# Kernel optimization log

Hardware: AMD Instinct MI355X
Metric: run time of the kernel (lower is better)

Reference implementation:

```python
import jax, jax.numpy as jnp
import numpy as np


def _apply_1q_batched(state, gate, q):
    # state: (B,2,2,2,2) complex; gate: (B,2,2) complex; acts on qubit q
    state = jnp.moveaxis(state, q + 1, -1)
    state = jnp.einsum('bij,b...j->b...i', gate, state)
    return jnp.moveaxis(state, -1, q + 1)


def _apply_cnot(state, c, t):
    # flip target bit where control bit == 1
    s0, s1 = jnp.split(state, 2, axis=c + 1)
    s1 = jnp.flip(s1, axis=t + 1)
    return jnp.concatenate([s0, s1], axis=c + 1)


def _quantum_features(angles, params):
    # angles: (B,4) RY rotation angles; params: (4,) RZ angles
    B = angles.shape[0]
    state = jnp.zeros((B, 16), jnp.complex64).at[:, 0].set(1.0).reshape(B, 2, 2, 2, 2)
    # RY(x_i) on each wire (batched angle per sample)
    for q in range(4):
        th = 0.5 * angles[:, q]
        c, s = jnp.cos(th), jnp.sin(th)
        gate = jnp.stack([jnp.stack([c, -s], -1), jnp.stack([s, c], -1)], -2).astype(jnp.complex64)
        state = _apply_1q_batched(state, gate, q)
    # RZ(params[i]) on wire i followed by CNOT(i, (i+1)%4), interleaved as in source
    pc = params.astype(jnp.complex64)
    for q in range(4):
        ph = jnp.exp(jnp.array([-0.5j, 0.5j], jnp.complex64) * pc[q])
        shp = [1, 1, 1, 1, 1]
        shp[q + 1] = 2
        state = state * ph.reshape(shp)
        state = _apply_cnot(state, q, (q + 1) % 4)
    probs = state.real ** 2 + state.imag ** 2  # (B,2,2,2,2)
    feats = []
    for q in range(4):
        axes = tuple(a for a in range(1, 5) if a != q + 1)
        p = probs.sum(axes)  # (B,2)
        feats.append(p[:, 0] - p[:, 1])  # <Z_q>
    return jnp.stack(feats, -1)  # (B,4)


def _deconv2x2(x, w, b):
    # PyTorch ConvTranspose2d with kernel=stride=2, padding=0 (non-overlapping)
    # x: (B,Ci,H,W), w: (Ci,Co,2,2), b: (Co,)
    B, Ci, H, W = x.shape
    Co = w.shape[1]
    y = jnp.einsum('bchw,codk->bohdwk', x, w).reshape(B, Co, 2 * H, 2 * W)
    return y + b[None, :, None, None]


def setup_inputs() -> dict:
    key = jax.random.key(0)
    ks = jax.random.split(key, 10)
    B = 16384
    return {
        'x': jax.random.uniform(ks[0], (B, 1, 28, 28), jnp.float32),
        'var_params': jax.random.normal(ks[1], (4,), jnp.float32),
        'w_lat': jax.random.normal(ks[2], (224, 4), jnp.float32) * 0.3,
        'b_lat': jax.random.normal(ks[3], (224,), jnp.float32) * 0.05,
        'w_fc': jax.random.normal(ks[4], (392, 224), jnp.float32) * 0.05,
        'b_fc': jax.random.normal(ks[5], (392,), jnp.float32) * 0.05,
        'w_d1': jax.random.normal(ks[6], (8, 4, 2, 2), jnp.float32) * 0.2,
        'b_d1': jax.random.normal(ks[7], (4,), jnp.float32) * 0.05,
        'w_d2': jax.random.normal(ks[8], (4, 1, 2, 2), jnp.float32) * 0.2,
        'b_d2': jax.random.normal(ks[9], (1,), jnp.float32) * 0.05,
    }


def reference(x, var_params, w_lat, b_lat, w_fc, b_fc, w_d1, b_d1, w_d2, b_d2):
    # quadrant means -> 4 angles per sample
    quad = jnp.stack([
        x[:, 0, :14, :14].mean((1, 2)),
        x[:, 0, :14, 14:].mean((1, 2)),
        x[:, 0, 14:, :14].mean((1, 2)),
        x[:, 0, 14:, 14:].mean((1, 2)),
    ], axis=1)  # (B,4)
    qf = _quantum_features(quad, var_params)  # (B,4)
    latent = jax.nn.relu(qf @ w_lat.T + b_lat)  # (B,224)
    h = jax.nn.relu(latent @ w_fc.T + b_fc)  # (B,392)
    h = h.reshape(-1, 8, 7, 7)
    h = jax.nn.relu(_deconv2x2(h, w_d1, b_d1))  # (B,4,14,14)
    out = jax.nn.sigmoid(_deconv2x2(h, w_d2, b_d2))  # (B,1,28,28)
    return out
```

## Files before the change

kernel.cpp:

```cpp
#include <hip/hip_runtime.h>
#include <math.h>

#define G 16
#define HS 396
#define LSTR 232

typedef __attribute__((ext_vector_type(8))) __bf16 bf16x8;
typedef __attribute__((ext_vector_type(4))) float f32x4;
typedef __attribute__((ext_vector_type(2))) float f32x2;

__global__ void wconv_kernel(const float* __restrict__ w_fc, __bf16* __restrict__ wb) {
  int tile = blockIdx.x;
  int kt   = blockIdx.y;
  int lane = threadIdx.x;
  int n  = tile * 16 + (lane & 15);
  int k0 = kt * 32 + (lane >> 4) * 8;
  bf16x8 v;
  if (n < 392) {
    const float* src = w_fc + (size_t)n * 224 + k0;
    float4 f0 = *(const float4*)(src);
    float4 f1 = *(const float4*)(src + 4);
    v[0] = (__bf16)f0.x; v[1] = (__bf16)f0.y; v[2] = (__bf16)f0.z; v[3] = (__bf16)f0.w;
    v[4] = (__bf16)f1.x; v[5] = (__bf16)f1.y; v[6] = (__bf16)f1.z; v[7] = (__bf16)f1.w;
  } else {
    #pragma unroll
    for (int j = 0; j < 8; ++j) v[j] = (__bf16)0.f;
  }
  *(bf16x8*)(wb + ((size_t)(tile * 7 + kt) * 64 + lane) * 8) = v;
}

__global__ __launch_bounds__(256, 4) void fused_kernel(
    const float* __restrict__ x, const float* __restrict__ params,
    const __bf16* __restrict__ wb,
    const float* __restrict__ w_lat, const float* __restrict__ b_lat,
    const float* __restrict__ b_fc,
    const float* __restrict__ w_d1, const float* __restrict__ b_d1,
    const float* __restrict__ w_d2, const float* __restrict__ b_d2,
    float* __restrict__ out, int B)
{
  __shared__ __align__(16) __bf16 latb[G * LSTR];
  __shared__ __align__(16) float hbuf[G * HS];
  __shared__ float qfs[G * 4];
  __shared__ float wd1[128];
  __shared__ float wd2[16];
  __shared__ float bd1[4];
  const int t = threadIdx.x;
  const int wv = t >> 6;
  const int lane = t & 63;
  const int s0g = blockIdx.x * G;
  if (s0g >= B) return;

  if (t < 128) wd1[t] = w_d1[t];
  else if (t < 144) wd2[t - 128] = w_d2[t - 128];
  else if (t < 148) bd1[t - 144] = b_d1[t - 144];

  {
    const float* xb = x + (size_t)(s0g + wv * 4) * 784;
    float acc[4][4];
    #pragma unroll
    for (int i = 0; i < 4; ++i)
      #pragma unroll
      for (int q = 0; q < 4; ++q) acc[i][q] = 0.f;
    for (int i4 = lane; i4 < 196; i4 += 64) {
      int base = i4 * 4;
      int r = base / 28;
      int cb = base - r * 28;
      float bt = (r >= 14) ? 1.f : 0.f;
      float tp = 1.f - bt;
      float w0[4], w1[4], w2[4], w3[4];
      #pragma unroll
      for (int e = 0; e < 4; ++e) {
        float lf = ((cb + e) < 14) ? 1.f : 0.f;
        float rf = 1.f - lf;
        w0[e] = tp * lf; w1[e] = tp * rf; w2[e] = bt * lf; w3[e] = bt * rf;
      }
      #pragma unroll
      for (int smp = 0; smp < 4; ++smp) {
        f32x4 v = __builtin_nontemporal_load((const f32x4*)(xb + smp * 784 + base));
        #pragma unroll
        for (int e = 0; e < 4; ++e) {
          acc[smp][0] = fmaf(v[e], w0[e], acc[smp][0]);
          acc[smp][1] = fmaf(v[e], w1[e], acc[smp][1]);
          acc[smp][2] = fmaf(v[e], w2[e], acc[smp][2]);
          acc[smp][3] = fmaf(v[e], w3[e], acc[smp][3]);
        }
      }
    }
    #pragma unroll
    for (int smp = 0; smp < 4; ++smp)
      #pragma unroll
      for (int q = 0; q < 4; ++q)
        #pragma unroll
        for (int o = 32; o > 0; o >>= 1)
          acc[smp][q] += __shfl_down(acc[smp][q], o, 64);
    if (lane == 0) {
      const float inv = 1.f / 196.f;
      #pragma unroll
      for (int smp = 0; smp < 4; ++smp) {
        float4 o;
        o.x = acc[smp][0] * inv; o.y = acc[smp][1] * inv;
        o.z = acc[smp][2] * inv; o.w = acc[smp][3] * inv;
        *(float4*)(qfs + (wv * 4 + smp) * 4) = o;
      }
    }
  }
  __syncthreads();

  if (t < G) {
    float means[4] = {qfs[t * 4], qfs[t * 4 + 1], qfs[t * 4 + 2], qfs[t * 4 + 3]};
    float cs[4], sn[4];
    #pragma unroll
    for (int q = 0; q < 4; ++q) {
      float th = 0.5f * means[q];
      sn[q] = __sinf(th);
      cs[q] = __cosf(th);
    }
    float re[16], im[16];
    #pragma unroll
    for (int idx = 0; idx < 16; ++idx) {
      float a = ((idx >> 3) & 1) ? sn[0] : cs[0];
      a *= ((idx >> 2) & 1) ? sn[1] : cs[1];
      a *= ((idx >> 1) & 1) ? sn[2] : cs[2];
      a *= (idx & 1) ? sn[3] : cs[3];
      re[idx] = a;
      im[idx] = 0.f;
    }
    #pragma unroll
    for (int q = 0; q < 4; ++q) {
      float hp = 0.5f * params[q];
      float sp = __sinf(hp), cp = __cosf(hp);
      int qb = 3 - q;
      #pragma unroll
      for (int idx = 0; idx < 16; ++idx) {
        float sg = ((idx >> qb) & 1) ? sp : -sp;
        float r0 = re[idx], i0 = im[idx];
        re[idx] = r0 * cp - i0 * sg;
        im[idx] = r0 * sg + i0 * cp;
      }
      int cm = 1 << qb;
      int tm = 1 << (3 - ((q + 1) & 3));
      #pragma unroll
      for (int idx = 0; idx < 16; ++idx) {
        if ((idx & cm) && !(idx & tm)) {
          int j = idx | tm;
          float tr = re[idx]; re[idx] = re[j]; re[j] = tr;
          float ti = im[idx]; im[idx] = im[j]; im[j] = ti;
        }
      }
    }
    #pragma unroll
    for (int q = 0; q < 4; ++q) {
      int qb = 3 - q;
      float z = 0.f;
      #pragma unroll
      for (int idx = 0; idx < 16; ++idx) {
        float p = re[idx] * re[idx] + im[idx] * im[idx];
        z += ((idx >> qb) & 1) ? -p : p;
      }
      qfs[t * 4 + q] = z;
    }
  }
  __syncthreads();

  for (int v = t; v < G * 224; v += 256) {
    int s = v / 224;
    int j = v - s * 224;
    float4 w = *(const float4*)(w_lat + j * 4);
    float a = b_lat[j];
    a = fmaf(qfs[s * 4 + 0], w.x, a);
    a = fmaf(qfs[s * 4 + 1], w.y, a);
    a = fmaf(qfs[s * 4 + 2], w.z, a);
    a = fmaf(qfs[s * 4 + 3], w.w, a);
    latb[s * LSTR + j] = (__bf16)fmaxf(a, 0.f);
  }
  __syncthreads();

  {
    const int m = lane & 15;
    const int kq = lane >> 4;
    const __bf16* arow = latb + m * LSTR + kq * 8;
    for (int tile = wv; tile < 25; tile += 4) {
      f32x4 acc = {0.f, 0.f, 0.f, 0.f};
      const bf16x8* bp = (const bf16x8*)(wb + ((size_t)(tile * 7) * 64 + lane) * 8);
      #pragma unroll
      for (int kt = 0; kt < 7; ++kt) {
        bf16x8 a = *(const bf16x8*)(arow + kt * 32);
        bf16x8 b = bp[kt * 64];
        acc = __builtin_amdgcn_mfma_f32_16x16x32_bf16(a, b, acc, 0, 0, 0);
      }
      int j = tile * 16 + m;
      if (j < 392) {
        float bf = b_fc[j];
        #pragma unroll
        for (int r = 0; r < 4; ++r)
          hbuf[(kq * 4 + r) * HS + j] = fmaxf(acc[r] + bf, 0.f);
      }
    }
  }
  __syncthreads();

  const float bd2v = b_d2[0];
  for (int v = t; v < G * 196; v += 256) {
    int s = v / 196;
    int p = v - s * 196;
    int Y = p / 14;
    int X = p - Y * 14;
    int y = Y >> 1, ey = Y & 1, xx = X >> 1, ex = X & 1;
    const float* hs = hbuf + s * HS + y * 7 + xx;
    float hv[8];
    #pragma unroll
    for (int ci = 0; ci < 8; ++ci) hv[ci] = hs[ci * 49];
    float o1[4];
    #pragma unroll
    for (int co = 0; co < 4; ++co) {
      float a = bd1[co];
      #pragma unroll
      for (int ci = 0; ci < 8; ++ci)
        a = fmaf(hv[ci], wd1[ci * 16 + co * 4 + ey * 2 + ex], a);
      o1[co] = fmaxf(a, 0.f);
    }
    size_t basep = (size_t)(s0g + s) * 784;
    #pragma unroll
    for (int dy = 0; dy < 2; ++dy) {
      float v0 = bd2v, v1 = bd2v;
      #pragma unroll
      for (int co = 0; co < 4; ++co) {
        v0 = fmaf(o1[co], wd2[co * 4 + dy * 2 + 0], v0);
        v1 = fmaf(o1[co], wd2[co * 4 + dy * 2 + 1], v1);
      }
      f32x2 o;
      o[0] = 1.f / (1.f + __expf(-v0));
      o[1] = 1.f / (1.f + __expf(-v1));
      __builtin_nontemporal_store(o, (f32x2*)(out + basep + (size_t)(2 * Y + dy) * 28 + 2 * X));
    }
  }
}

extern "C" void kernel_launch(void* const* d_in, const int* in_sizes, int n_in,
                              void* d_out, int out_size, void* d_ws, size_t ws_size,
                              hipStream_t stream) {
  const float* x          = (const float*)d_in[0];
  const float* var_params = (const float*)d_in[1];
  const float* w_lat      = (const float*)d_in[2];
  const float* b_lat      = (const float*)d_in[3];
  const float* w_fc       = (const float*)d_in[4];
  const float* b_fc       = (const float*)d_in[5];
  const float* w_d1       = (const float*)d_in[6];
  const float* b_d1       = (const float*)d_in[7];
  const float* w_d2       = (const float*)d_in[8];
  const float* b_d2       = (const float*)d_in[9];
  float* out = (float*)d_out;

  __bf16* wb = (__bf16*)d_ws;

  int B = in_sizes[0] / 784;
  wconv_kernel<<<dim3(25, 7), 64, 0, stream>>>(w_fc, wb);
  fused_kernel<<<(B + G - 1) / G, 256, 0, stream>>>(
      x, var_params, wb, w_lat, b_lat, b_fc, w_d1, b_d1, w_d2, b_d2, out, B);
}
```

Before: 143.9 us.

## Parallelize quantum sim across lanes, drop barriers, store hidden as bf16

Simulates the 4-qubit circuit with 16 lanes per sample: one amplitude per lane, CNOTs done as shuffles and expectations as xor-reductions. Previously only 16 threads did this serially. Each wave now handles its own 4 samples end to end through the latent layer, which removes two block-wide barriers. The hidden buffer becomes bf16 and launch bounds rise to 6 blocks per CU, cutting LDS use to raise occupancy. This costs some precision in the deconvolution inputs and may force register spills under the tighter bound.

```diff
diff --git a/kernel.cpp b/kernel.cpp
--- a/kernel.cpp
+++ b/kernel.cpp
@@ -2,7 +2,7 @@
 #include <math.h>
 
 #define G 16
-#define HS 396
+#define HS2 400
 #define LSTR 232
 
 typedef __attribute__((ext_vector_type(8))) __bf16 bf16x8;
@@ -29,7 +29,7 @@
   *(bf16x8*)(wb + ((size_t)(tile * 7 + kt) * 64 + lane) * 8) = v;
 }
 
-__global__ __launch_bounds__(256, 4) void fused_kernel(
+__global__ __launch_bounds__(256, 6) void fused_kernel(
     const float* __restrict__ x, const float* __restrict__ params,
     const __bf16* __restrict__ wb,
     const float* __restrict__ w_lat, const float* __restrict__ b_lat,
@@ -39,8 +39,8 @@
     float* __restrict__ out, int B)
 {
   __shared__ __align__(16) __bf16 latb[G * LSTR];
-  __shared__ __align__(16) float hbuf[G * HS];
-  __shared__ float qfs[G * 4];
+  __shared__ __align__(16) __bf16 hbuf[G * HS2];
+  __shared__ __align__(16) float qfs[G * 4];
   __shared__ float wd1[128];
   __shared__ float wd2[16];
   __shared__ float bd1[4];
@@ -104,74 +104,67 @@
       }
     }
   }
-  __syncthreads();
-
-  if (t < G) {
-    float means[4] = {qfs[t * 4], qfs[t * 4 + 1], qfs[t * 4 + 2], qfs[t * 4 + 3]};
-    float cs[4], sn[4];
-    #pragma unroll
-    for (int q = 0; q < 4; ++q) {
-      float th = 0.5f * means[q];
-      sn[q] = __sinf(th);
-      cs[q] = __cosf(th);
-    }
-    float re[16], im[16];
-    #pragma unroll
-    for (int idx = 0; idx < 16; ++idx) {
-      float a = ((idx >> 3) & 1) ? sn[0] : cs[0];
-      a *= ((idx >> 2) & 1) ? sn[1] : cs[1];
-      a *= ((idx >> 1) & 1) ? sn[2] : cs[2];
-      a *= (idx & 1) ? sn[3] : cs[3];
-      re[idx] = a;
-      im[idx] = 0.f;
-    }
+
+  {
+    const int sub = lane >> 4;
+    const int i   = lane & 15;
+    const int s   = wv * 4 + sub;
+    float4 mn = *(const float4*)(qfs + s * 4);
+    float c_[4], s_[4];
+    c_[0] = __cosf(0.5f * mn.x); s_[0] = __sinf(0.5f * mn.x);
+    c_[1] = __cosf(0.5f * mn.y); s_[1] = __sinf(0.5f * mn.y);
+    c_[2] = __cosf(0.5f * mn.z); s_[2] = __sinf(0.5f * mn.z);
+    c_[3] = __cosf(0.5f * mn.w); s_[3] = __sinf(0.5f * mn.w);
+    float re = (((i >> 3) & 1) ? s_[0] : c_[0]) * (((i >> 2) & 1) ? s_[1] : c_[1])
+             * (((i >> 1) & 1) ? s_[2] : c_[2]) * ((i & 1) ? s_[3] : c_[3]);
+    float im = 0.f;
     #pragma unroll
     for (int q = 0; q < 4; ++q) {
       float hp = 0.5f * params[q];
       float sp = __sinf(hp), cp = __cosf(hp);
       int qb = 3 - q;
-      #pragma unroll
-      for (int idx = 0; idx < 16; ++idx) {
-        float sg = ((idx >> qb) & 1) ? sp : -sp;
-        float r0 = re[idx], i0 = im[idx];
-        re[idx] = r0 * cp - i0 * sg;
-        im[idx] = r0 * sg + i0 * cp;
-      }
+      float sg = ((i >> qb) & 1) ? sp : -sp;
+      float r0 = re, i0 = im;
+      re = r0 * cp - i0 * sg;
+      im = r0 * sg + i0 * cp;
       int cm = 1 << qb;
       int tm = 1 << (3 - ((q + 1) & 3));
-      #pragma unroll
-      for (int idx = 0; idx < 16; ++idx) {
-        if ((idx & cm) && !(idx & tm)) {
-          int j = idx | tm;
-          float tr = re[idx]; re[idx] = re[j]; re[j] = tr;
-          float ti = im[idx]; im[idx] = im[j]; im[j] = ti;
-        }
-      }
-    }
+      int srcI = (i & cm) ? (i ^ tm) : i;
+      int srcLane = (lane & ~15) | srcI;
+      re = __shfl(re, srcLane, 64);
+      im = __shfl(im, srcLane, 64);
+    }
+    float p = re * re + im * im;
+    float z[4];
     #pragma unroll
     for (int q = 0; q < 4; ++q) {
       int qb = 3 - q;
-      float z = 0.f;
-      #pragma unroll
-      for (int idx = 0; idx < 16; ++idx) {
-        float p = re[idx] * re[idx] + im[idx] * im[idx];
-        z += ((idx >> qb) & 1) ? -p : p;
-      }
-      qfs[t * 4 + q] = z;
-    }
-  }
-  __syncthreads();
-
-  for (int v = t; v < G * 224; v += 256) {
-    int s = v / 224;
-    int j = v - s * 224;
-    float4 w = *(const float4*)(w_lat + j * 4);
-    float a = b_lat[j];
-    a = fmaf(qfs[s * 4 + 0], w.x, a);
-    a = fmaf(qfs[s * 4 + 1], w.y, a);
-    a = fmaf(qfs[s * 4 + 2], w.z, a);
-    a = fmaf(qfs[s * 4 + 3], w.w, a);
-    latb[s * LSTR + j] = (__bf16)fmaxf(a, 0.f);
+      float v = ((i >> qb) & 1) ? -p : p;
+      v += __shfl_xor(v, 1, 16);
+      v += __shfl_xor(v, 2, 16);
+      v += __shfl_xor(v, 4, 16);
+      v += __shfl_xor(v, 8, 16);
+      z[q] = v;
+    }
+    if (i < 4) {
+      float zv = (i == 0) ? z[0] : (i == 1) ? z[1] : (i == 2) ? z[2] : z[3];
+      qfs[s * 4 + i] = zv;
+    }
+  }
+
+  #pragma unroll
+  for (int sl = 0; sl < 4; ++sl) {
+    int s = wv * 4 + sl;
+    float4 q4 = *(const float4*)(qfs + s * 4);
+    for (int j = lane; j < 224; j += 64) {
+      float4 w = *(const float4*)(w_lat + j * 4);
+      float a = b_lat[j];
+      a = fmaf(q4.x, w.x, a);
+      a = fmaf(q4.y, w.y, a);
+      a = fmaf(q4.z, w.z, a);
+      a = fmaf(q4.w, w.w, a);
+      latb[s * LSTR + j] = (__bf16)fmaxf(a, 0.f);
+    }
   }
   __syncthreads();
 
@@ -193,7 +186,7 @@
         float bf = b_fc[j];
         #pragma unroll
         for (int r = 0; r < 4; ++r)
-          hbuf[(kq * 4 + r) * HS + j] = fmaxf(acc[r] + bf, 0.f);
+          hbuf[(kq * 4 + r) * HS2 + j] = (__bf16)fmaxf(acc[r] + bf, 0.f);
       }
     }
   }
@@ -206,10 +199,10 @@
     int Y = p / 14;
     int X = p - Y * 14;
     int y = Y >> 1, ey = Y & 1, xx = X >> 1, ex = X & 1;
-    const float* hs = hbuf + s * HS + y * 7 + xx;
+    const __bf16* hs = hbuf + s * HS2 + y * 7 + xx;
     float hv[8];
     #pragma unroll
-    for (int ci = 0; ci < 8; ++ci) hv[ci] = hs[ci * 49];
+    for (int ci = 0; ci < 8; ++ci) hv[ci] = (float)hs[ci * 49];
     float o1[4];
     #pragma unroll
     for (int co = 0; co < 4; ++co) {
```

Result: no change. 145.0 us (+0.8%).
